# Optimization experiments

Measured on AMD Instinct MI355X. Metric: run time of the kernel, lower is better.

Reference implementation:

```python
import jax, jax.numpy as jnp
import numpy as np

HID = 512
HEADS = 8
PF = 2048
EPS = 1e-5


def _layernorm(x, g, b):
    mu = jnp.mean(x, axis=-1, keepdims=True)
    var = jnp.var(x, axis=-1, keepdims=True)
    return (x - mu) * jax.lax.rsqrt(var + EPS) * g + b


def setup_inputs() -> dict:
    key = jax.random.key(0)
    ks = jax.random.split(key, 20)
    s = 0.02
    inp = {
        "trg": jax.random.normal(ks[0], (16, 1024, HID), jnp.float32),
        "src": jax.random.normal(ks[1], (16, 1024, HID), jnp.float32),
        "ln_g": jnp.ones((HID,), jnp.float32),
        "ln_b": jnp.zeros((HID,), jnp.float32),
        "wq": jax.random.normal(ks[2], (HID, HID), jnp.float32) * s,
        "bq": jnp.zeros((HID,), jnp.float32),
        "wk": jax.random.normal(ks[3], (HID, HID), jnp.float32) * s,
        "bk": jnp.zeros((HID,), jnp.float32),
        "wv": jax.random.normal(ks[4], (HID, HID), jnp.float32) * s,
        "bv": jnp.zeros((HID,), jnp.float32),
        "wo": jax.random.normal(ks[5], (HID, HID), jnp.float32) * s,
        "bo": jnp.zeros((HID,), jnp.float32),
        "pf1_w": jax.random.normal(ks[6], (PF, HID), jnp.float32) * s,
        "pf1_b": jnp.zeros((PF,), jnp.float32),
        "pf2_w": jax.random.normal(ks[7], (HID, PF), jnp.float32) * s,
        "pf2_b": jnp.zeros((HID,), jnp.float32),
        "fc1_w": jax.random.normal(ks[8], (256, HID), jnp.float32) * s,
        "fc1_b": jnp.zeros((256,), jnp.float32),
        "fc2_w": jax.random.normal(ks[9], (2, 256), jnp.float32) * s,
        "fc2_b": jnp.zeros((2,), jnp.float32),
    }
    return inp


def reference(trg, src, ln_g, ln_b, wq, bq, wk, bk, wv, bv, wo, bo,
              pf1_w, pf1_b, pf2_w, pf2_b, fc1_w, fc1_b, fc2_w, fc2_b):
    B, T, D = trg.shape
    S = src.shape[1]
    dh = D // HEADS

    # --- multi-head attention (Q=trg, K=V=src, no mask; dropout=eval/no-op) ---
    q = (trg @ wq.T + bq).reshape(B, T, HEADS, dh)
    k = (src @ wk.T + bk).reshape(B, S, HEADS, dh)
    v = (src @ wv.T + bv).reshape(B, S, HEADS, dh)
    scores = jnp.einsum('bqhd,bkhd->bhqk', q, k) / jnp.sqrt(jnp.float32(dh))
    attn = jax.nn.softmax(scores, axis=-1)
    ctx = jnp.einsum('bhqk,bkhd->bqhd', attn, v).reshape(B, T, D)
    sa_out = ctx @ wo.T + bo

    x = _layernorm(trg + sa_out, ln_g, ln_b)

    # --- position-wise feed-forward ---
    h = jax.nn.relu(x @ pf1_w.T + pf1_b)
    ff = h @ pf2_w.T + pf2_b
    x = _layernorm(x + ff, ln_g, ln_b)

    # --- norm-weighted sum pooling over sequence (vectorized) ---
    norm = jnp.linalg.norm(x, axis=2)              # [B, T]
    w = jax.nn.softmax(norm, axis=1)               # [B, T]
    pooled = jnp.einsum('bt,btd->bd', w, x)        # [B, D]

    label = jax.nn.relu(pooled @ fc1_w.T + fc1_b) @ fc2_w.T + fc2_b
    return label
```

## Files before the change

### kernel.cpp

```cpp
#include <hip/hip_runtime.h>

typedef __bf16 bf16x8 __attribute__((ext_vector_type(8)));
typedef float f32x4 __attribute__((ext_vector_type(4)));
typedef unsigned short u16;

__device__ __forceinline__ u16 f2bf(float f){
  unsigned u = __builtin_bit_cast(unsigned, f);
  u += 0x7fffu + ((u>>16)&1u);
  return (u16)(u>>16);
}
__device__ __forceinline__ float bf2f(u16 h){
  unsigned u = ((unsigned)h)<<16; return __builtin_bit_cast(float,u);
}
__device__ __forceinline__ bf16x8 ld8(const u16* p){ return *(const bf16x8*)p; }
__device__ __forceinline__ f32x4 mfma16(bf16x8 a, bf16x8 b, f32x4 c){
  return __builtin_amdgcn_mfma_f32_16x16x32_bf16(a,b,c,0,0,0);
}
__device__ __forceinline__ void gl16(const u16* g, u16* l){
  __builtin_amdgcn_global_load_lds(
    (const __attribute__((address_space(1))) unsigned int*)g,
    (__attribute__((address_space(3))) unsigned int*)l, 16, 0, 0);
}
__device__ __forceinline__ unsigned cvtpk(float a, float b){
  unsigned r;
  asm("v_cvt_pk_bf16_f32 %0, %1, %2" : "=v"(r) : "v"(a), "v"(b));
  return r;
}

#define QSC 0.18033688f

__global__ __launch_bounds__(256) void k_split2(const float* __restrict__ a,
    const float* __restrict__ b, u16* __restrict__ da, u16* __restrict__ db, int n){
  const float* s = blockIdx.y ? b : a;
  u16* d = blockIdx.y ? db : da;
  int i = (blockIdx.x*256 + threadIdx.x)*4;
  const int stride = gridDim.x*256*4;
  for(; i<n; i+=stride){
    float4 v = *(const float4*)(s+i);
    ushort4 H = {f2bf(v.x),f2bf(v.y),f2bf(v.z),f2bf(v.w)};
    *(ushort4*)(d+i)=H;
  }
}

struct SplitW { const float* s[6]; u16* d[6]; int n[6]; };
__global__ __launch_bounds__(256) void k_splitw(SplitW P){
  const int y = blockIdx.y;
  const float* s = P.s[y]; u16* d = P.d[y]; const int n = P.n[y];
  int i = (blockIdx.x*256 + threadIdx.x)*4;
  const int stride = gridDim.x*256*4;
  for(; i<n; i+=stride){
    float4 v = *(const float4*)(s+i);
    ushort4 H = {f2bf(v.x),f2bf(v.y),f2bf(v.z),f2bf(v.w)};
    *(ushort4*)(d+i)=H;
  }
}

template<int EPI>
__global__ __launch_bounds__(512) void k_gemm(
  const u16* __restrict__ A, const u16* __restrict__ W,
  const float* __restrict__ bias, int M, int N, int K,
  float* __restrict__ Cf, u16* __restrict__ Oh)
{
  __shared__ __align__(16) u16 sA[2][128*64], sW[2][128*64];
  const int tid = threadIdx.x, w = tid>>6, l = tid&63;
  const int l15 = l&15, g = l>>4;
  const int gx = gridDim.x;
  const int bid = blockIdx.y*gx + blockIdx.x;
  const int nwg = gx*gridDim.y;
  const int wgid = (bid&7)*(nwg>>3) + (bid>>3);
  const int m0 = (wgid/gx)*128, n0 = (wgid%gx)*128;
  const int wm = w>>2, wn = w&3;
  f32x4 acc[4][2] = {};
  const int wrow = w*16;
  const int sr = l>>3, sslot = l&7;
  int scolA[2];
  #pragma unroll
  for(int i=0;i<2;i++){
    const int R = wrow + i*8 + sr;
    scolA[i] = 8*((sslot - ((R>>1)&7)) & 7);
  }
  int offA[4][2], offW[2][2];
  #pragma unroll
  for(int i=0;i<4;i++){
    const int R = wm*64+i*16+l15;
    #pragma unroll
    for(int kk=0;kk<2;kk++) offA[i][kk] = R*64 + (((g+4*kk)+((R>>1)&7))&7)*8;
  }
  #pragma unroll
  for(int j=0;j<2;j++){
    const int C = wn*32+j*16+l15;
    #pragma unroll
    for(int kk=0;kk<2;kk++) offW[j][kk] = C*64 + (((g+4*kk)+((C>>1)&7))&7)*8;
  }
  const u16* Ab = A + (long)m0*K;
  const u16* Wb = W + (long)n0*K;
  const int nk = K>>6;

#define G_STAGE(BUF, T) { \
    const int k0 = (T)<<6; \
    _Pragma("unroll") \
    for(int i=0;i<2;i++){ \
      const int rows = wrow + i*8; \
      gl16(Ab + (long)(rows+sr)*K + k0 + scolA[i], sA[BUF] + rows*64); \
      gl16(Wb + (long)(rows+sr)*K + k0 + scolA[i], sW[BUF] + rows*64); \
    } }

#define G_STEP(CUR, T) { \
    if((T)+1 < nk) G_STAGE(CUR^1, (T)+1); \
    _Pragma("unroll") \
    for(int kk=0;kk<2;kk++){ \
      bf16x8 av[4], wv[2]; \
      _Pragma("unroll") for(int i=0;i<4;i++) av[i] = *(const bf16x8*)(sA[CUR]+offA[i][kk]); \
      _Pragma("unroll") for(int j=0;j<2;j++) wv[j] = *(const bf16x8*)(sW[CUR]+offW[j][kk]); \
      _Pragma("unroll") for(int j=0;j<2;j++){ \
        _Pragma("unroll") for(int i=0;i<4;i++) acc[i][j] = mfma16(av[i], wv[j], acc[i][j]); } \
    } \
    __syncthreads(); }

  G_STAGE(0,0); __syncthreads();
  for(int t=0;t<nk;t+=2){ G_STEP(0,t); G_STEP(1,t+1); }
#undef G_STAGE
#undef G_STEP

  #pragma unroll
  for(int i=0;i<4;i++){
    #pragma unroll
    for(int j=0;j<2;j++){
      const int col  = n0 + wn*32 + j*16 + l15;
      const float bb = bias ? bias[col] : 0.f;
      const int rowb = m0 + wm*64 + i*16 + g*4;
      #pragma unroll
      for(int jj=0;jj<4;jj++){
        float v = acc[i][j][jj] + bb;
        const int row = rowb + jj;
        if constexpr(EPI==0){ Cf[(long)row*N + col] = v; }
        else if constexpr(EPI==1){ Oh[(long)row*N + col] = f2bf(v); }
        else { Oh[(long)row*N + col] = f2bf(fmaxf(v,0.f)); }
      }
    }
  }
}

__global__ __launch_bounds__(512) void k_qkv(
  const u16* __restrict__ trg_hi, const u16* __restrict__ src_hi,
  const u16* __restrict__ Wh,
  const float* __restrict__ bq, const float* __restrict__ bk, const float* __restrict__ bv,
  u16* __restrict__ Qb, u16* __restrict__ Kb, u16* __restrict__ Vt)
{
  __shared__ __align__(16) u16 sA[2][128*64], sW[2][128*64];
  const int tid = threadIdx.x, w = tid>>6, l = tid&63;
  const int l15 = l&15, g = l>>4;
  const int bid = blockIdx.x;
  const int wgid = (bid&7)*192 + (bid>>3);
  const int m0 = (wgid/12)*128, n0 = (wgid%12)*128;
  const u16* A = (n0<512)? trg_hi : src_hi;
  const float* bp = (n0<512)? bq : (n0<1024? bk : bv);
  const int nb = (n0<512)? 0 : (n0<1024? 512 : 1024);
  const int wm = w>>2, wn = w&3;
  f32x4 acc[4][2] = {};
  const int wrow = w*16;
  const int sr = l>>3, sslot = l&7;
  int scolA[2];
  #pragma unroll
  for(int i=0;i<2;i++){
    const int R = wrow + i*8 + sr;
    scolA[i] = 8*((sslot - ((R>>1)&7)) & 7);
  }
  int offA[4][2], offW[2][2];
  #pragma unroll
  for(int i=0;i<4;i++){
    const int R = wm*64+i*16+l15;
    #pragma unroll
    for(int kk=0;kk<2;kk++) offA[i][kk] = R*64 + (((g+4*kk)+((R>>1)&7))&7)*8;
  }
  #pragma unroll
  for(int j=0;j<2;j++){
    const int C = wn*32+j*16+l15;
    #pragma unroll
    for(int kk=0;kk<2;kk++) offW[j][kk] = C*64 + (((g+4*kk)+((C>>1)&7))&7)*8;
  }
  const u16* Ab = A  + (long)m0*512;
  const u16* Wb = Wh + (long)n0*512;

#define Q_STAGE(BUF, T) { \
    const int k0 = (T)<<6; \
    _Pragma("unroll") \
    for(int i=0;i<2;i++){ \
      const int rows = wrow + i*8; \
      gl16(Ab + (long)(rows+sr)*512 + k0 + scolA[i], sA[BUF] + rows*64); \
      gl16(Wb + (long)(rows+sr)*512 + k0 + scolA[i], sW[BUF] + rows*64); \
    } }

#define Q_STEP(CUR, T) { \
    if((T)+1 < 8) Q_STAGE(CUR^1, (T)+1); \
    _Pragma("unroll") \
    for(int kk=0;kk<2;kk++){ \
      bf16x8 av[4], wv[2]; \
      _Pragma("unroll") for(int i=0;i<4;i++) av[i] = *(const bf16x8*)(sA[CUR]+offA[i][kk]); \
      _Pragma("unroll") for(int j=0;j<2;j++) wv[j] = *(const bf16x8*)(sW[CUR]+offW[j][kk]); \
      _Pragma("unroll") for(int j=0;j<2;j++){ \
        _Pragma("unroll") for(int i=0;i<4;i++) acc[i][j] = mfma16(av[i], wv[j], acc[i][j]); } \
    } \
    __syncthreads(); }

  Q_STAGE(0,0); __syncthreads();
  for(int t=0;t<8;t+=2){ Q_STEP(0,t); Q_STEP(1,t+1); }
#undef Q_STAGE
#undef Q_STEP

  #pragma unroll
  for(int i=0;i<4;i++){
    #pragma unroll
    for(int j=0;j<2;j++){
      const int col = n0 + wn*32 + j*16 + l15;
      const int cl  = col - nb;
      const float bb = bp[cl];
      const int rowb = m0 + wm*64 + i*16 + g*4;
      #pragma unroll
      for(int jj=0;jj<4;jj++){
        float v = acc[i][j][jj] + bb;
        const int row = rowb + jj;
        if(n0 < 512){ Qb[(long)row*512 + cl] = f2bf(v*QSC); }
        else if(n0 < 1024){ Kb[(long)row*512 + cl] = f2bf(v); }
        else {
          const int h = cl>>6, d = cl&63;
          const long dst = (((long)(row>>10)*8 + h)*64 + d)*1024
                         + ((row>>6)&15)*64 + (row&15)*4 + ((row>>4)&3);
          Vt[dst] = f2bf(v);
        }
      }
    }
  }
}

__global__ __launch_bounds__(512) void k_attn(
  const u16* __restrict__ Q, const u16* __restrict__ K,
  const u16* __restrict__ Vt, u16* __restrict__ O)
{
  __shared__ __align__(16) u16 sK[64*64], sV[64*64];
  __shared__ __align__(16) u16 Ph[8][16*72];
  const int bid = blockIdx.x;
  const int wg = (bid&7)*128 + (bid>>3);
  const int q0 = (wg&7)*128, hd = (wg>>3)&7, b = wg>>6;
  const int tid = threadIdx.x, w = tid>>6, l = tid&63, l15 = l&15, g = l>>4;
  const int qrow = q0 + w*16 + l15;
  const long qoff = (long)(b*1024 + qrow)*512 + hd*64 + g*8;
  bf16x8 qf[2] = { ld8(Q+qoff), ld8(Q+qoff+32) };
  const int srw = l>>3, sslot = l&7;
  const int scol = 8*(sslot ^ srw);
  const int rows = w*8;
  const u16* Kb = K + (long)b*1024*512 + hd*64;
  const u16* Vb = Vt + (long)(b*8+hd)*64*1024;
  f32x4 rs = {};
  f32x4 ctx[4] = {};
  for(int s0=0;s0<1024;s0+=64){
    gl16(Kb + (long)(s0+rows+srw)*512 + scol, sK + rows*64);
    gl16(Vb + (long)(rows+srw)*1024 + s0 + scol, sV + rows*64);
    __syncthreads();
    f32x4 sv[4];
    #pragma unroll
    for(int sf=0;sf<4;sf++){
      const int row = sf*16 + l15;
      f32x4 a = {};
      #pragma unroll
      for(int h=0;h<2;h++){
        const int ch = (g + 4*h) ^ (row&7);
        a = mfma16(qf[h], *(const bf16x8*)(sK + row*64 + ch*8), a);
      }
      sv[sf] = a;
    }
    float p[4][4];
    #pragma unroll
    for(int sf=0;sf<4;sf++){
      #pragma unroll
      for(int j=0;j<4;j++){
        p[sf][j] = exp2f(sv[sf][j]);
        rs[j] += p[sf][j];
      }
    }
    #pragma unroll
    for(int j=0;j<4;j++){
      uint2 pk = { cvtpk(p[0][j], p[1][j]), cvtpk(p[2][j], p[3][j]) };
      *(uint2*)(&Ph[w][(g*4+j)*72 + l15*4]) = pk;
    }
    #pragma unroll
    for(int ss=0;ss<2;ss++){
      bf16x8 pa = *(const bf16x8*)(&Ph[w][l15*72 + ss*32 + g*8]);
      #pragma unroll
      for(int df=0;df<4;df++){
        const int row = df*16 + l15;
        const int ch = (ss*4 + g) ^ (row&7);
        ctx[df] = mfma16(pa, *(const bf16x8*)(sV + row*64 + ch*8), ctx[df]);
      }
    }
    __syncthreads();
  }
  float inv[4];
  #pragma unroll
  for(int j=0;j<4;j++){
    float t = rs[j];
    #pragma unroll
    for(int mask=1;mask<16;mask<<=1) t += __shfl_xor(t, mask);
    inv[j] = 1.f/t;
  }
  #pragma unroll
  for(int df=0;df<4;df++){
    #pragma unroll
    for(int j=0;j<4;j++){
      const float v = ctx[df][j] * inv[j];
      const long off = (long)(b*1024 + q0 + w*16 + g*4 + j)*512 + hd*64 + df*16 + l15;
      O[off] = f2bf(v);
    }
  }
}

template<int XAF>
__global__ __launch_bounds__(256) void k_ln(
  const float* __restrict__ xaf, const u16* __restrict__ xab,
  const u16* __restrict__ xbb,
  const float* __restrict__ gg, const float* __restrict__ bvec,
  u16* __restrict__ yh, float* __restrict__ norms)
{
  const int w = threadIdx.x>>6, l = threadIdx.x&63;
  const long rrow = (long)blockIdx.x*4 + w;
  const long base = rrow*512 + l*8;
  float va[8];
  if constexpr(XAF){
    float4 a0 = *(const float4*)(xaf+base), a1 = *(const float4*)(xaf+base+4);
    va[0]=a0.x; va[1]=a0.y; va[2]=a0.z; va[3]=a0.w;
    va[4]=a1.x; va[5]=a1.y; va[6]=a1.z; va[7]=a1.w;
  } else {
    ushort4 a0 = *(const ushort4*)(xab+base), a1 = *(const ushort4*)(xab+base+4);
    va[0]=bf2f(a0.x); va[1]=bf2f(a0.y); va[2]=bf2f(a0.z); va[3]=bf2f(a0.w);
    va[4]=bf2f(a1.x); va[5]=bf2f(a1.y); va[6]=bf2f(a1.z); va[7]=bf2f(a1.w);
  }
  ushort4 b0 = *(const ushort4*)(xbb+base), b1 = *(const ushort4*)(xbb+base+4);
  float v[8] = {va[0]+bf2f(b0.x), va[1]+bf2f(b0.y), va[2]+bf2f(b0.z), va[3]+bf2f(b0.w),
                va[4]+bf2f(b1.x), va[5]+bf2f(b1.y), va[6]+bf2f(b1.z), va[7]+bf2f(b1.w)};
  float s=0.f, q=0.f;
  #pragma unroll
  for(int j=0;j<8;j++){ s += v[j]; q += v[j]*v[j]; }
  #pragma unroll
  for(int mask=1;mask<64;mask<<=1){ s += __shfl_xor(s,mask); q += __shfl_xor(q,mask); }
  const float mu  = s*(1.f/512.f);
  const float var = q*(1.f/512.f) - mu*mu;
  const float rstd = rsqrtf(var + 1e-5f);
  float y[8]; float nq = 0.f;
  #pragma unroll
  for(int j=0;j<8;j++){
    const int c = l*8+j;
    y[j] = (v[j]-mu)*rstd*gg[c] + bvec[c];
    nq += y[j]*y[j];
  }
  u16 hv[8];
  #pragma unroll
  for(int j=0;j<8;j++){ hv[j]=f2bf(y[j]); }
  ushort4 hh0={hv[0],hv[1],hv[2],hv[3]}, hh1={hv[4],hv[5],hv[6],hv[7]};
  *(ushort4*)(yh+base)=hh0; *(ushort4*)(yh+base+4)=hh1;
  if(norms){
    #pragma unroll
    for(int mask=1;mask<64;mask<<=1) nq += __shfl_xor(nq,mask);
    if(l==0) norms[rrow] = sqrtf(nq);
  }
}

__global__ __launch_bounds__(256) void k_pool2(const u16* __restrict__ x2,
   const float* __restrict__ norms, float* __restrict__ partial)
{
  const int b = blockIdx.y, tc = blockIdx.z;
  const int col = blockIdx.x*256 + threadIdx.x;
  __shared__ float wsm[1024];
  __shared__ float red[4];
  const int tid = threadIdx.x, w = tid>>6, l = tid&63;
  float lm = -1e30f;
  for(int i=tid;i<1024;i+=256){ const float n = norms[b*1024+i]; wsm[i]=n; lm=fmaxf(lm,n); }
  #pragma unroll
  for(int mask=1;mask<64;mask<<=1) lm = fmaxf(lm, __shfl_xor(lm,mask));
  __syncthreads();
  if(l==0) red[w]=lm;
  __syncthreads();
  const float bm = fmaxf(fmaxf(red[0],red[1]), fmaxf(red[2],red[3]));
  __syncthreads();
  float ls = 0.f;
  for(int i=tid;i<1024;i+=256){ const float e = __expf(wsm[i]-bm); wsm[i]=e; ls+=e; }
  #pragma unroll
  for(int mask=1;mask<64;mask<<=1) ls += __shfl_xor(ls,mask);
  __syncthreads();
  if(l==0) red[w]=ls;
  __syncthreads();
  const float inv = 1.f/(red[0]+red[1]+red[2]+red[3]);
  float acc = 0.f;
  const int t0 = tc*128;
  for(int t=t0;t<t0+128;t++) acc += wsm[t]*bf2f(x2[((long)b*1024+t)*512 + col]);
  partial[((long)tc*16 + b)*512 + col] = acc*inv;
}

__global__ __launch_bounds__(256) void k_poolr(const float* __restrict__ partial,
   float* __restrict__ pooled)
{
  const int i = blockIdx.x*256 + threadIdx.x;
  float a = 0.f;
  #pragma unroll
  for(int tc=0;tc<8;tc++) a += partial[tc*8192 + i];
  pooled[i] = a;
}

__global__ __launch_bounds__(256) void k_head(const float* __restrict__ pooled,
  const float* __restrict__ w1, const float* __restrict__ b1,
  const float* __restrict__ w2, const float* __restrict__ b2,
  float* __restrict__ out)
{
  __shared__ float ps[16*512];
  __shared__ float h1[16*256];
  const int tid = threadIdx.x;
  for(int i=tid;i<16*512;i+=256) ps[i]=pooled[i];
  __syncthreads();
  float acc[16] = {};
  for(int k=0;k<512;k++){
    const float wv = w1[tid*512+k];
    #pragma unroll
    for(int i=0;i<16;i++) acc[i] += ps[i*512+k]*wv;
  }
  #pragma unroll
  for(int i=0;i<16;i++) h1[i*256+tid] = fmaxf(acc[i]+b1[tid], 0.f);
  __syncthreads();
  if(tid<32){
    const int i = tid>>1, o = tid&1;
    float a = b2[o];
    for(int k=0;k<256;k++) a += h1[i*256+k]*w2[o*256+k];
    out[i*2+o] = a;
  }
}

extern "C" void kernel_launch(void* const* d_in, const int* in_sizes, int n_in,
                              void* d_out, int out_size, void* d_ws, size_t ws_size,
                              hipStream_t stream)
{
  const float* trg  = (const float*)d_in[0];
  const float* src  = (const float*)d_in[1];
  const float* ln_g = (const float*)d_in[2];
  const float* ln_b = (const float*)d_in[3];
  const float* wq   = (const float*)d_in[4];  const float* bq  = (const float*)d_in[5];
  const float* wk   = (const float*)d_in[6];  const float* bk  = (const float*)d_in[7];
  const float* wv   = (const float*)d_in[8];  const float* bv  = (const float*)d_in[9];
  const float* wo   = (const float*)d_in[10]; const float* bo  = (const float*)d_in[11];
  const float* pf1w = (const float*)d_in[12]; const float* pf1b= (const float*)d_in[13];
  const float* pf2w = (const float*)d_in[14]; const float* pf2b= (const float*)d_in[15];
  const float* fc1w = (const float*)d_in[16]; const float* fc1b= (const float*)d_in[17];
  const float* fc2w = (const float*)d_in[18]; const float* fc2b= (const float*)d_in[19];
  float* out = (float*)d_out;

  char* ws = (char*)d_ws;
  const size_t PL = (size_t)16384*512*2;
  auto P = [&](int i)->u16*{ return (u16*)(ws + (size_t)i*PL); };
  u16 *Qb=P(0), *Kb=P(1), *Vt=P(2), *ctx=P(3);
  u16 *trg_hi=P(4), *src_hi=P(5);
  u16 *sa_bf = P(4);
  u16 *x1_hi = P(5);
  u16 *h_hi  = P(0);
  u16 *ffb_bf= P(4);
  u16 *x2_bf = P(6);
  size_t off = 7*PL;
  auto carve = [&](size_t n)->char*{ char* p = ws+off; off += n; return p; };
  u16* wqkv_hi=(u16*)carve((size_t)1536*512*2);
  u16* wo_hi=(u16*)carve(512*512*2);
  u16* p1_hi=(u16*)carve((size_t)2048*512*2);
  u16* p2_hi=(u16*)carve((size_t)512*2048*2);
  float* norms  = (float*)carve(16384*4);
  float* partial= (float*)carve(8*16*512*4);
  float* pooled = (float*)carve(16*512*4);
  (void)ws_size; (void)in_sizes; (void)n_in; (void)out_size;

  const int NTOK = 16384;

  k_split2<<<dim3(8192,2),256,0,stream>>>(trg, src, trg_hi, src_hi, NTOK*512);
  SplitW sw;
  sw.s[0]=wq;  sw.d[0]=wqkv_hi;           sw.n[0]=512*512;
  sw.s[1]=wk;  sw.d[1]=wqkv_hi+512*512;   sw.n[1]=512*512;
  sw.s[2]=wv;  sw.d[2]=wqkv_hi+1024*512;  sw.n[2]=512*512;
  sw.s[3]=wo;  sw.d[3]=wo_hi;             sw.n[3]=512*512;
  sw.s[4]=pf1w; sw.d[4]=p1_hi;            sw.n[4]=2048*512;
  sw.s[5]=pf2w; sw.d[5]=p2_hi;            sw.n[5]=512*2048;
  k_splitw<<<dim3(512,6),256,0,stream>>>(sw);

  k_qkv<<<dim3(1536),512,0,stream>>>(trg_hi,src_hi,wqkv_hi,bq,bk,bv,Qb,Kb,Vt);

  k_attn<<<dim3(1024),512,0,stream>>>(Qb,Kb,Vt,ctx);

  k_gemm<1><<<dim3(4,128),512,0,stream>>>(ctx,wo_hi,bo,NTOK,512,512,nullptr,sa_bf);
  k_ln<1><<<dim3(4096),256,0,stream>>>(trg, nullptr, sa_bf, ln_g, ln_b, x1_hi, nullptr);

  k_gemm<2><<<dim3(16,128),512,0,stream>>>(x1_hi,p1_hi,pf1b,NTOK,2048,512,nullptr,h_hi);
  k_gemm<1><<<dim3(4,128),512,0,stream>>>(h_hi,p2_hi,pf2b,NTOK,512,2048,nullptr,ffb_bf);
  k_ln<0><<<dim3(4096),256,0,stream>>>(nullptr, x1_hi, ffb_bf, ln_g, ln_b, x2_bf, norms);

  k_pool2<<<dim3(2,16,8),256,0,stream>>>(x2_bf, norms, partial);
  k_poolr<<<dim3(32),256,0,stream>>>(partial, pooled);
  k_head<<<1,256,0,stream>>>(pooled, fc1w, fc1b, fc2w, fc2b, out);
}
```

Before: 308.6 us.

## Switch GEMMs to 32x32x16 MFMA and merge conversion kernels into one launch

The GEMM and QKV kernels now use the 32x32x16 bf16 MFMA instruction, with two 32x32 accumulators per wave in place of eight 16x16 tiles. This cuts the number of MFMA issues and LDS fragment reads per k-step, and the epilogue index mapping is rewritten to match. Separately, the activation and weight fp32-to-bf16 conversions are merged into a single 8-way launch. The merged launch uses fewer blocks for the large activation arrays, which may leave the bandwidth-bound conversion under-occupied.

```diff
diff --git a/kernel.cpp b/kernel.cpp
--- a/kernel.cpp
+++ b/kernel.cpp
@@ -2,6 +2,7 @@
 
 typedef __bf16 bf16x8 __attribute__((ext_vector_type(8)));
 typedef float f32x4 __attribute__((ext_vector_type(4)));
+typedef float f32x16 __attribute__((ext_vector_type(16)));
 typedef unsigned short u16;
 
 __device__ __forceinline__ u16 f2bf(float f){
@@ -16,6 +17,9 @@
 __device__ __forceinline__ f32x4 mfma16(bf16x8 a, bf16x8 b, f32x4 c){
   return __builtin_amdgcn_mfma_f32_16x16x32_bf16(a,b,c,0,0,0);
 }
+__device__ __forceinline__ f32x16 mfma32(bf16x8 a, bf16x8 b, f32x16 c){
+  return __builtin_amdgcn_mfma_f32_32x32x16_bf16(a,b,c,0,0,0);
+}
 __device__ __forceinline__ void gl16(const u16* g, u16* l){
   __builtin_amdgcn_global_load_lds(
     (const __attribute__((address_space(1))) unsigned int*)g,
@@ -29,21 +33,8 @@
 
 #define QSC 0.18033688f
 
-__global__ __launch_bounds__(256) void k_split2(const float* __restrict__ a,
-    const float* __restrict__ b, u16* __restrict__ da, u16* __restrict__ db, int n){
-  const float* s = blockIdx.y ? b : a;
-  u16* d = blockIdx.y ? db : da;
-  int i = (blockIdx.x*256 + threadIdx.x)*4;
-  const int stride = gridDim.x*256*4;
-  for(; i<n; i+=stride){
-    float4 v = *(const float4*)(s+i);
-    ushort4 H = {f2bf(v.x),f2bf(v.y),f2bf(v.z),f2bf(v.w)};
-    *(ushort4*)(d+i)=H;
-  }
-}
-
-struct SplitW { const float* s[6]; u16* d[6]; int n[6]; };
-__global__ __launch_bounds__(256) void k_splitw(SplitW P){
+struct Split8 { const float* s[8]; u16* d[8]; int n[8]; };
+__global__ __launch_bounds__(256) void k_split8(Split8 P){
   const int y = blockIdx.y;
   const float* s = P.s[y]; u16* d = P.d[y]; const int n = P.n[y];
   int i = (blockIdx.x*256 + threadIdx.x)*4;
@@ -63,14 +54,14 @@
 {
   __shared__ __align__(16) u16 sA[2][128*64], sW[2][128*64];
   const int tid = threadIdx.x, w = tid>>6, l = tid&63;
-  const int l15 = l&15, g = l>>4;
+  const int l31 = l&31, half = l>>5;
   const int gx = gridDim.x;
   const int bid = blockIdx.y*gx + blockIdx.x;
   const int nwg = gx*gridDim.y;
   const int wgid = (bid&7)*(nwg>>3) + (bid>>3);
   const int m0 = (wgid/gx)*128, n0 = (wgid%gx)*128;
   const int wm = w>>2, wn = w&3;
-  f32x4 acc[4][2] = {};
+  f32x16 acc[2] = {};
   const int wrow = w*16;
   const int sr = l>>3, sslot = l&7;
   int scolA[2];
@@ -79,18 +70,17 @@
     const int R = wrow + i*8 + sr;
     scolA[i] = 8*((sslot - ((R>>1)&7)) & 7);
   }
-  int offA[4][2], offW[2][2];
-  #pragma unroll
-  for(int i=0;i<4;i++){
-    const int R = wm*64+i*16+l15;
-    #pragma unroll
-    for(int kk=0;kk<2;kk++) offA[i][kk] = R*64 + (((g+4*kk)+((R>>1)&7))&7)*8;
-  }
-  #pragma unroll
-  for(int j=0;j<2;j++){
-    const int C = wn*32+j*16+l15;
-    #pragma unroll
-    for(int kk=0;kk<2;kk++) offW[j][kk] = C*64 + (((g+4*kk)+((C>>1)&7))&7)*8;
+  int offA[2][4], offW[4];
+  #pragma unroll
+  for(int i=0;i<2;i++){
+    const int R = wm*64 + i*32 + l31;
+    #pragma unroll
+    for(int ks=0;ks<4;ks++) offA[i][ks] = R*64 + (((ks*2+half)+((R>>1)&7))&7)*8;
+  }
+  {
+    const int C = wn*32 + l31;
+    #pragma unroll
+    for(int ks=0;ks<4;ks++) offW[ks] = C*64 + (((ks*2+half)+((C>>1)&7))&7)*8;
   }
   const u16* Ab = A + (long)m0*K;
   const u16* Wb = W + (long)n0*K;
@@ -108,12 +98,10 @@
 #define G_STEP(CUR, T) { \
     if((T)+1 < nk) G_STAGE(CUR^1, (T)+1); \
     _Pragma("unroll") \
-    for(int kk=0;kk<2;kk++){ \
-      bf16x8 av[4], wv[2]; \
-      _Pragma("unroll") for(int i=0;i<4;i++) av[i] = *(const bf16x8*)(sA[CUR]+offA[i][kk]); \
-      _Pragma("unroll") for(int j=0;j<2;j++) wv[j] = *(const bf16x8*)(sW[CUR]+offW[j][kk]); \
-      _Pragma("unroll") for(int j=0;j<2;j++){ \
-        _Pragma("unroll") for(int i=0;i<4;i++) acc[i][j] = mfma16(av[i], wv[j], acc[i][j]); } \
+    for(int ks=0;ks<4;ks++){ \
+      bf16x8 bv = *(const bf16x8*)(sW[CUR]+offW[ks]); \
+      acc[0] = mfma32(*(const bf16x8*)(sA[CUR]+offA[0][ks]), bv, acc[0]); \
+      acc[1] = mfma32(*(const bf16x8*)(sA[CUR]+offA[1][ks]), bv, acc[1]); \
     } \
     __syncthreads(); }
 
@@ -122,21 +110,17 @@
 #undef G_STAGE
 #undef G_STEP
 
-  #pragma unroll
-  for(int i=0;i<4;i++){
-    #pragma unroll
-    for(int j=0;j<2;j++){
-      const int col  = n0 + wn*32 + j*16 + l15;
-      const float bb = bias ? bias[col] : 0.f;
-      const int rowb = m0 + wm*64 + i*16 + g*4;
-      #pragma unroll
-      for(int jj=0;jj<4;jj++){
-        float v = acc[i][j][jj] + bb;
-        const int row = rowb + jj;
-        if constexpr(EPI==0){ Cf[(long)row*N + col] = v; }
-        else if constexpr(EPI==1){ Oh[(long)row*N + col] = f2bf(v); }
-        else { Oh[(long)row*N + col] = f2bf(fmaxf(v,0.f)); }
-      }
+  const int col = n0 + wn*32 + l31;
+  const float bb = bias ? bias[col] : 0.f;
+  #pragma unroll
+  for(int i=0;i<2;i++){
+    #pragma unroll
+    for(int r=0;r<16;r++){
+      const int row = m0 + wm*64 + i*32 + (r&3) + 8*(r>>2) + 4*half;
+      float v = acc[i][r] + bb;
+      if constexpr(EPI==0){ Cf[(long)row*N + col] = v; }
+      else if constexpr(EPI==1){ Oh[(long)row*N + col] = f2bf(v); }
+      else { Oh[(long)row*N + col] = f2bf(fmaxf(v,0.f)); }
     }
   }
 }
@@ -149,7 +133,7 @@
 {
   __shared__ __align__(16) u16 sA[2][128*64], sW[2][128*64];
   const int tid = threadIdx.x, w = tid>>6, l = tid&63;
-  const int l15 = l&15, g = l>>4;
+  const int l31 = l&31, half = l>>5;
   const int bid = blockIdx.x;
   const int wgid = (bid&7)*192 + (bid>>3);
   const int m0 = (wgid/12)*128, n0 = (wgid%12)*128;
@@ -157,7 +141,7 @@
   const float* bp = (n0<512)? bq : (n0<1024? bk : bv);
   const int nb = (n0<512)? 0 : (n0<1024? 512 : 1024);
   const int wm = w>>2, wn = w&3;
-  f32x4 acc[4][2] = {};
+  f32x16 acc[2] = {};
   const int wrow = w*16;
   const int sr = l>>3, sslot = l&7;
   int scolA[2];
@@ -166,18 +150,17 @@
     const int R = wrow + i*8 + sr;
     scolA[i] = 8*((sslot - ((R>>1)&7)) & 7);
   }
-  int offA[4][2], offW[2][2];
-  #pragma unroll
-  for(int i=0;i<4;i++){
-    const int R = wm*64+i*16+l15;
-    #pragma unroll
-    for(int kk=0;kk<2;kk++) offA[i][kk] = R*64 + (((g+4*kk)+((R>>1)&7))&7)*8;
-  }
-  #pragma unroll
-  for(int j=0;j<2;j++){
-    const int C = wn*32+j*16+l15;
-    #pragma unroll
-    for(int kk=0;kk<2;kk++) offW[j][kk] = C*64 + (((g+4*kk)+((C>>1)&7))&7)*8;
+  int offA[2][4], offW[4];
+  #pragma unroll
+  for(int i=0;i<2;i++){
+    const int R = wm*64 + i*32 + l31;
+    #pragma unroll
+    for(int ks=0;ks<4;ks++) offA[i][ks] = R*64 + (((ks*2+half)+((R>>1)&7))&7)*8;
+  }
+  {
+    const int C = wn*32 + l31;
+    #pragma unroll
+    for(int ks=0;ks<4;ks++) offW[ks] = C*64 + (((ks*2+half)+((C>>1)&7))&7)*8;
   }
   const u16* Ab = A  + (long)m0*512;
   const u16* Wb = Wh + (long)n0*512;
@@ -194,12 +177,10 @@
 #define Q_STEP(CUR, T) { \
     if((T)+1 < 8) Q_STAGE(CUR^1, (T)+1); \
     _Pragma("unroll") \
-    for(int kk=0;kk<2;kk++){ \
-      bf16x8 av[4], wv[2]; \
-      _Pragma("unroll") for(int i=0;i<4;i++) av[i] = *(const bf16x8*)(sA[CUR]+offA[i][kk]); \
-      _Pragma("unroll") for(int j=0;j<2;j++) wv[j] = *(const bf16x8*)(sW[CUR]+offW[j][kk]); \
-      _Pragma("unroll") for(int j=0;j<2;j++){ \
-        _Pragma("unroll") for(int i=0;i<4;i++) acc[i][j] = mfma16(av[i], wv[j], acc[i][j]); } \
+    for(int ks=0;ks<4;ks++){ \
+      bf16x8 bv = *(const bf16x8*)(sW[CUR]+offW[ks]); \
+      acc[0] = mfma32(*(const bf16x8*)(sA[CUR]+offA[0][ks]), bv, acc[0]); \
+      acc[1] = mfma32(*(const bf16x8*)(sA[CUR]+offA[1][ks]), bv, acc[1]); \
     } \
     __syncthreads(); }
 
@@ -208,26 +189,22 @@
 #undef Q_STAGE
 #undef Q_STEP
 
-  #pragma unroll
-  for(int i=0;i<4;i++){
-    #pragma unroll
-    for(int j=0;j<2;j++){
-      const int col = n0 + wn*32 + j*16 + l15;
-      const int cl  = col - nb;
-      const float bb = bp[cl];
-      const int rowb = m0 + wm*64 + i*16 + g*4;
-      #pragma unroll
-      for(int jj=0;jj<4;jj++){
-        float v = acc[i][j][jj] + bb;
-        const int row = rowb + jj;
-        if(n0 < 512){ Qb[(long)row*512 + cl] = f2bf(v*QSC); }
-        else if(n0 < 1024){ Kb[(long)row*512 + cl] = f2bf(v); }
-        else {
-          const int h = cl>>6, d = cl&63;
-          const long dst = (((long)(row>>10)*8 + h)*64 + d)*1024
-                         + ((row>>6)&15)*64 + (row&15)*4 + ((row>>4)&3);
-          Vt[dst] = f2bf(v);
-        }
+  const int col = n0 + wn*32 + l31;
+  const int cl  = col - nb;
+  const float bb = bp[cl];
+  #pragma unroll
+  for(int i=0;i<2;i++){
+    #pragma unroll
+    for(int r=0;r<16;r++){
+      const int row = m0 + wm*64 + i*32 + (r&3) + 8*(r>>2) + 4*half;
+      float v = acc[i][r] + bb;
+      if(n0 < 512){ Qb[(long)row*512 + cl] = f2bf(v*QSC); }
+      else if(n0 < 1024){ Kb[(long)row*512 + cl] = f2bf(v); }
+      else {
+        const int h = cl>>6, d = cl&63;
+        const long dst = (((long)(row>>10)*8 + h)*64 + d)*1024
+                       + ((row>>6)&15)*64 + (row&15)*4 + ((row>>4)&3);
+        Vt[dst] = f2bf(v);
       }
     }
   }
@@ -473,15 +450,16 @@
 
   const int NTOK = 16384;
 
-  k_split2<<<dim3(8192,2),256,0,stream>>>(trg, src, trg_hi, src_hi, NTOK*512);
-  SplitW sw;
-  sw.s[0]=wq;  sw.d[0]=wqkv_hi;           sw.n[0]=512*512;
-  sw.s[1]=wk;  sw.d[1]=wqkv_hi+512*512;   sw.n[1]=512*512;
-  sw.s[2]=wv;  sw.d[2]=wqkv_hi+1024*512;  sw.n[2]=512*512;
-  sw.s[3]=wo;  sw.d[3]=wo_hi;             sw.n[3]=512*512;
-  sw.s[4]=pf1w; sw.d[4]=p1_hi;            sw.n[4]=2048*512;
-  sw.s[5]=pf2w; sw.d[5]=p2_hi;            sw.n[5]=512*2048;
-  k_splitw<<<dim3(512,6),256,0,stream>>>(sw);
+  Split8 sp;
+  sp.s[0]=trg;  sp.d[0]=trg_hi;           sp.n[0]=NTOK*512;
+  sp.s[1]=src;  sp.d[1]=src_hi;           sp.n[1]=NTOK*512;
+  sp.s[2]=wq;   sp.d[2]=wqkv_hi;          sp.n[2]=512*512;
+  sp.s[3]=wk;   sp.d[3]=wqkv_hi+512*512;  sp.n[3]=512*512;
+  sp.s[4]=wv;   sp.d[4]=wqkv_hi+1024*512; sp.n[4]=512*512;
+  sp.s[5]=wo;   sp.d[5]=wo_hi;            sp.n[5]=512*512;
+  sp.s[6]=pf1w; sp.d[6]=p1_hi;            sp.n[6]=2048*512;
+  sp.s[7]=pf2w; sp.d[7]=p2_hi;            sp.n[7]=512*2048;
+  k_split8<<<dim3(1024,8),256,0,stream>>>(sp);
 
   k_qkv<<<dim3(1536),512,0,stream>>>(trg_hi,src_hi,wqkv_hi,bq,bk,bv,Qb,Kb,Vt);
 
```

Measured after the change: 304.3 us. No clear change (-1.4%).
